# Kernel tuning notes

Measured on AMD Instinct MI355X. Metric: run time of the kernel, lower is better.

Reference implementation:

```python
import jax
import jax.numpy as jnp
import numpy as np
from jax import lax

KSIZE = 3
C = 32


def _conv3x3(x, w):
    # NCHW input, OIHW weight, stride 1, padding 1 (matches nn.Conv2d(padding=1))
    return lax.conv_general_dilated(
        x, w, window_strides=(1, 1), padding=((1, 1), (1, 1)),
        dimension_numbers=("NCHW", "OIHW", "NCHW"))


def setup_inputs() -> dict:
    key = jax.random.key(0)
    k1, k2, k3 = jax.random.split(key, 3)
    N, H, W = 2, 64, 64
    x = jax.random.normal(k1, (N, C, H, W), dtype=jnp.float32)
    # conv1: C -> C, 3x3; PyTorch default init scale ~ 1/sqrt(fan_in)
    conv1_w = jax.random.normal(k2, (C, C, 3, 3), dtype=jnp.float32) * (1.0 / np.sqrt(C * 9))
    # conv2: C -> C*C*9, 3x3
    conv2_w = jax.random.normal(k3, (C * C * KSIZE * KSIZE, C, 3, 3), dtype=jnp.float32) * (1.0 / np.sqrt(C * 9))
    return {"x": x, "conv1_w": conv1_w, "conv2_w": conv2_w}


def reference(x, conv1_w, conv2_w):
    N, _, H, W = x.shape
    # kernel-generation branch: conv -> relu -> conv -> tanh
    h = jax.nn.relu(_conv3x3(x, conv1_w))
    rst = _conv3x3(h, conv2_w)  # [N, C*C*9, H, W]
    weight = jnp.tanh(rst.reshape(N, C, C, H, W, KSIZE, KSIZE))
    # non-uniform conv apply: per-pixel CxC 3x3 kernel, pad=1
    xp = jnp.pad(x, ((0, 0), (0, 0), (1, 1), (1, 1)))
    # patches[n, ci, h, w, kh, kw] = xp[n, ci, h+kh, w+kw]
    patches = jnp.stack(
        [xp[:, :, kh:kh + H, kw:kw + W] for kh in range(KSIZE) for kw in range(KSIZE)],
        axis=-1).reshape(N, C, H, W, KSIZE, KSIZE)
    out = jnp.einsum("noihwkl,nihwkl->nohw", weight, patches)
    return out
```

## Files before the change

kernel.cpp:

```cpp
#include <hip/hip_runtime.h>

typedef unsigned int uint;
typedef unsigned short ushort_t;

#define CN 32
#define HW 4096
#define KDIM 288
#define PDIM 8192
#define NB 2

typedef __attribute__((ext_vector_type(8))) short bf16x8;
typedef __attribute__((ext_vector_type(4))) float f32x4;

static __device__ __forceinline__ ushort_t f2bf(float f) {
    uint u = __float_as_uint(f);
    uint r = (u + 0x7fffu + ((u >> 16) & 1u)) >> 16;
    return (ushort_t)r;
}

static __device__ __forceinline__ void gl_lds16(const void* g, void* l) {
    __builtin_amdgcn_global_load_lds(
        (const __attribute__((address_space(1))) unsigned int*)g,
        (__attribute__((address_space(3))) unsigned int*)l, 16, 0, 0);
}

static __device__ __forceinline__ float fast_tanh(float v) {
    float e = __expf(2.0f * v);
    return 1.0f - 2.0f * __builtin_amdgcn_rcpf(e + 1.0f);
}


__global__ __launch_bounds__(256) void prep_kernel(
    const float* __restrict__ x, const float* __restrict__ w1,
    const float* __restrict__ w2, float* __restrict__ hout,
    ushort_t* __restrict__ A_bf, float4* __restrict__ out_zero)
{
    __shared__ float w1s[KDIM];
    __shared__ float ps[2][128][4];
    int bb = blockIdx.x;
    int tid = threadIdx.x;
    if (bb < 512) {
        int n  = bb >> 8;
        int c  = (bb >> 3) & 31;
        int rg = bb & 7;
        for (int j = tid; j < KDIM; j += 256) w1s[j] = w1[c * KDIM + j];
        __syncthreads();

        int half = tid >> 7;
        int i2   = tid & 127;
        int hh   = rg * 8 + (i2 >> 4);
        int ws0  = (i2 & 15) * 4;

        float acc0 = 0.f, acc1 = 0.f, acc2 = 0.f, acc3 = 0.f;
        int ci0 = half * 16;
        for (int ci = ci0; ci < ci0 + 16; ci++) {
            const float* xp = x + (((size_t)(n * CN + ci)) << 12);
            #pragma unroll
            for (int kh = 0; kh < 3; kh++) {
                int y = hh + kh - 1;
                if ((unsigned)y >= 64u) continue;
                const float* row = xp + (y << 6);
                float4 v = *(const float4*)(row + ws0);
                float left  = (ws0 > 0)  ? row[ws0 - 1] : 0.f;
                float right = (ws0 < 60) ? row[ws0 + 4] : 0.f;
                float rb[6] = {left, v.x, v.y, v.z, v.w, right};
                const float* wp = &w1s[ci * 9 + kh * 3];
                #pragma unroll
                for (int kw = 0; kw < 3; kw++) {
                    float wgt = wp[kw];
                    acc0 = fmaf(wgt, rb[0 + kw], acc0);
                    acc1 = fmaf(wgt, rb[1 + kw], acc1);
                    acc2 = fmaf(wgt, rb[2 + kw], acc2);
                    acc3 = fmaf(wgt, rb[3 + kw], acc3);
                }
            }
        }
        ps[half][i2][0] = acc0; ps[half][i2][1] = acc1;
        ps[half][i2][2] = acc2; ps[half][i2][3] = acc3;
        __syncthreads();
        if (half == 0) {
            float4 o = make_float4(
                fmaxf(ps[0][i2][0] + ps[1][i2][0], 0.f),
                fmaxf(ps[0][i2][1] + ps[1][i2][1], 0.f),
                fmaxf(ps[0][i2][2] + ps[1][i2][2], 0.f),
                fmaxf(ps[0][i2][3] + ps[1][i2][3], 0.f));
            *(float4*)(hout + (((size_t)(n * CN + c)) << 12) + (hh << 6) + ws0) = o;
        }
    } else {
        int idx = (bb - 512) * 256 + tid;
        if (idx < 65536)
            out_zero[idx] = make_float4(0.f, 0.f, 0.f, 0.f);
        int row = idx / 36;
        int cw  = idx - row * 36;
        int g = cw >> 2, s = cw & 3;
        const float* base = w2 + (size_t)row * KDIM + g * 32;
        float4 lo = *(const float4*)(base + s * 4);
        float4 hi = *(const float4*)(base + 16 + s * 4);
        alignas(16) ushort_t o[8] = {f2bf(lo.x), f2bf(lo.y), f2bf(lo.z), f2bf(lo.w),
                                     f2bf(hi.x), f2bf(hi.y), f2bf(hi.z), f2bf(hi.w)};
        *(uint4*)(A_bf + (size_t)idx * 8) = *(const uint4*)o;
    }
}

__global__ __launch_bounds__(256) void im2col_bf16_perm(
    const float* __restrict__ h, ushort_t* __restrict__ Bm)
{
    int idx = blockIdx.x * 256 + threadIdx.x;
    int p  = idx / 36;
    int cw = idx - p * 36;
    int g = cw >> 2, s = cw & 3;
    int n  = p >> 12;
    int sp = p & 4095;
    int hh = sp >> 6;
    int w  = sp & 63;
    const float* hn = h + (((size_t)n * CN) << 12);
    alignas(16) ushort_t o[8];
    #pragma unroll
    for (int j = 0; j < 8; j++) {
        int ko = (j < 4) ? (s * 4 + j) : (12 + s * 4 + j);
        int k  = g * 32 + ko;
        int ci = (k * 57) >> 9;
        int kk = k - ci * 9;
        int kh = (kk * 11) >> 5;
        int kw = kk - kh * 3;
        int y  = hh + kh - 1;
        int xw = w + kw - 1;
        float v = 0.f;
        if ((unsigned)y < 64u && (unsigned)xw < 64u)
            v = hn[((size_t)ci << 12) + (y << 6) + xw];
        o[j] = f2bf(v);
    }
    *(uint4*)(Bm + (size_t)idx * 8) = *(const uint4*)o;
}

__global__ __launch_bounds__(512, 4) void fused_gemm_apply(
    const ushort_t* __restrict__ A, const ushort_t* __restrict__ B,
    const float* __restrict__ x, float* __restrict__ out)
{
    __shared__ ushort_t AL[3][128 * 32];
    __shared__ ushort_t BL[3][256 * 32];
    __shared__ float vred[4][256];

    int tid = threadIdx.x;
    int bid = blockIdx.x;
    int sb  = (bid & 7) * 288 + (bid >> 3);
    int tw  = sb % 144;
    int cg  = (sb / 144) & 7;
    int n   = sb / 1152;

    int lane = tid & 63, wv = tid >> 6;
    int wm = wv >> 2, wt = wv & 3;
    int i16 = lane & 15, kg = lane >> 4;

    int T0 = tw * 256;
    int c8 = T0 >> 12;
    int q0 = T0 & 4095;

    int cA = tid;
    int rA = cA >> 2;
    int k8A = (((cA & 3) ^ ((cA >> 3) & 3)) << 3);
    const ushort_t* srcA = A +
        (size_t)((cg * 4 + (rA >> 5)) * KDIM + (rA & 31) * 9 + c8) * KDIM + k8A;
    int cB0 = tid, cB1 = 512 + tid;
    int rB0 = cB0 >> 2, rB1 = cB1 >> 2;
    int k8B0 = (((cB0 & 3) ^ ((cB0 >> 3) & 3)) << 3);
    int k8B1 = (((cB1 & 3) ^ ((cB1 >> 3) & 3)) << 3);
    const ushort_t* srcB0 = B + (size_t)((n << 12) + q0 + rB0) * KDIM + k8B0;
    const ushort_t* srcB1 = B + (size_t)((n << 12) + q0 + rB1) * KDIM + k8B1;
    int dstA = wv * 512, dstB0 = wv * 512, dstB1 = 4096 + wv * 512;

#define STAGE(BUF, KS)                                                  \
    do { int _k0 = (KS) * 32;                                           \
        gl_lds16(srcA + _k0,  &AL[BUF][dstA]);                          \
        gl_lds16(srcB0 + _k0, &BL[BUF][dstB0]);                         \
        gl_lds16(srcB1 + _k0, &BL[BUF][dstB1]);                         \
    } while (0)

    f32x4 acc[4][4] = {};

    STAGE(0, 0);
    STAGE(1, 1);

    #pragma unroll
    for (int ks = 0; ks < 9; ks++) {
        int cur = ks % 3;
        if (ks < 7) {
            STAGE((ks + 2) % 3, ks + 2);
            __builtin_amdgcn_sched_barrier(0);
            asm volatile("s_waitcnt vmcnt(6)" ::: "memory");
        } else if (ks == 7) {
            __builtin_amdgcn_sched_barrier(0);
            asm volatile("s_waitcnt vmcnt(3)" ::: "memory");
        } else {
            __builtin_amdgcn_sched_barrier(0);
            asm volatile("s_waitcnt vmcnt(0)" ::: "memory");
        }
        __builtin_amdgcn_sched_barrier(0);
        __builtin_amdgcn_s_barrier();
        __builtin_amdgcn_sched_barrier(0);

        bf16x8 af[4], bfr[4];
        #pragma unroll
        for (int mf = 0; mf < 4; mf++) {
            int row = wm * 64 + mf * 16 + i16;
            af[mf] = *(const bf16x8*)
                &AL[cur][row * 32 + ((kg ^ ((row >> 1) & 3)) << 3)];
        }
        #pragma unroll
        for (int nf = 0; nf < 4; nf++) {
            int row = wt * 64 + nf * 16 + i16;
            bfr[nf] = *(const bf16x8*)
                &BL[cur][row * 32 + ((kg ^ ((row >> 1) & 3)) << 3)];
        }
        #pragma unroll
        for (int mf = 0; mf < 4; mf++)
            #pragma unroll
            for (int nf = 0; nf < 4; nf++)
                acc[mf][nf] = __builtin_amdgcn_mfma_f32_16x16x32_bf16(
                    af[mf], bfr[nf], acc[mf][nf], 0, 0, 0);

        __builtin_amdgcn_sched_barrier(0);
        asm volatile("s_waitcnt lgkmcnt(0)" ::: "memory");
        __builtin_amdgcn_sched_barrier(0);
        __builtin_amdgcn_s_barrier();
        __builtin_amdgcn_sched_barrier(0);
    }
#undef STAGE

    const float* xn = x + (((size_t)n * CN) << 12);
    #pragma unroll
    for (int nf = 0; nf < 4; nf++) {
        int t  = T0 + wt * 64 + nf * 16 + i16;
        uint sp = ((uint)t * 58255u) >> 19;
        int kk = t - (int)sp * 9;
        int kh = (kk * 11) >> 5;
        int kw = kk - kh * 3;
        int y  = (int)(sp >> 6) + kh - 1;
        int xw = (int)(sp & 63) + kw - 1;
        bool ok = ((unsigned)y < 64u) && ((unsigned)xw < 64u);
        int poff = (y << 6) + xw;
        float xa[4], xb[4];
        #pragma unroll
        for (int r = 0; r < 4; r++) {
            int cia = kg * 4 + r;
            xa[r] = ok ? xn[((size_t)cia << 12) + poff] : 0.f;
            xb[r] = ok ? xn[((size_t)(cia + 16) << 12) + poff] : 0.f;
        }
        float s0 = 0.f, s1 = 0.f;
        #pragma unroll
        for (int r = 0; r < 4; r++) {
            s0 = fmaf(fast_tanh(acc[0][nf][r]), xa[r], s0);
            s0 = fmaf(fast_tanh(acc[1][nf][r]), xb[r], s0);
            s1 = fmaf(fast_tanh(acc[2][nf][r]), xa[r], s1);
            s1 = fmaf(fast_tanh(acc[3][nf][r]), xb[r], s1);
        }
        s0 += __shfl_xor(s0, 16); s0 += __shfl_xor(s0, 32);
        s1 += __shfl_xor(s1, 16); s1 += __shfl_xor(s1, 32);
        if (kg == 0) {
            vred[2 * wm + 0][wt * 64 + nf * 16 + i16] = s0;
            vred[2 * wm + 1][wt * 64 + nf * 16 + i16] = s1;
        }
    }
    __syncthreads();

    if (tid < 128) {
        int g  = tid >> 5, bi = tid & 31;
        uint spA = ((uint)T0 * 58255u) >> 19;
        int sp = (int)spA + bi;
        int lo = sp * 9;     if (lo < T0) lo = T0;
        int hi = sp * 9 + 9; if (hi > T0 + 256) hi = T0 + 256;
        if (lo < hi) {
            float s = 0.f;
            for (int t = lo; t < hi; t++) s += vred[g][t - T0];
            atomicAdd(&out[(((size_t)n * CN + cg * 4 + g) << 12) + sp], s);
        }
    }
}

extern "C" void kernel_launch(void* const* d_in, const int* in_sizes, int n_in,
                              void* d_out, int out_size, void* d_ws, size_t ws_size,
                              hipStream_t stream) {
    const float* x  = (const float*)d_in[0];
    const float* w1 = (const float*)d_in[1];
    const float* w2 = (const float*)d_in[2];
    float* out = (float*)d_out;
    char* ws = (char*)d_ws;

    float*    hbuf  = (float*)ws;
    ushort_t* Bm_bf = (ushort_t*)(ws + 1048576u);
    ushort_t* A_bf  = (ushort_t*)(ws + 5767168u);

    hipLaunchKernelGGL(prep_kernel, dim3(1808), dim3(256), 0, stream,
                       x, w1, w2, hbuf, A_bf, (float4*)out);
    hipLaunchKernelGGL(im2col_bf16_perm, dim3(1152), dim3(256), 0,
                       stream, hbuf, Bm_bf);
    hipLaunchKernelGGL(fused_gemm_apply, dim3(2304), dim3(512), 0, stream,
                       A_bf, Bm_bf, x, out);
}
```

Baseline: 98.17 us.

## Restructure fused GEMM to 128x128 tiles with BK=64 split-phase double buffering

```diff
diff --git a/kernel.cpp b/kernel.cpp
--- a/kernel.cpp
+++ b/kernel.cpp
@@ -133,99 +133,159 @@
     *(uint4*)(Bm + (size_t)idx * 8) = *(const uint4*)o;
 }
 
-__global__ __launch_bounds__(512, 4) void fused_gemm_apply(
+__global__ __launch_bounds__(256) void fused_gemm_apply(
     const ushort_t* __restrict__ A, const ushort_t* __restrict__ B,
     const float* __restrict__ x, float* __restrict__ out)
 {
-    __shared__ ushort_t AL[3][128 * 32];
-    __shared__ ushort_t BL[3][256 * 32];
-    __shared__ float vred[4][256];
+    __shared__ ushort_t AL[2][128 * 64];
+    __shared__ ushort_t BL[2][128 * 64];
+    __shared__ float vred[4][128];
 
     int tid = threadIdx.x;
     int bid = blockIdx.x;
-    int sb  = (bid & 7) * 288 + (bid >> 3);
-    int tw  = sb % 144;
-    int cg  = (sb / 144) & 7;
-    int n   = sb / 1152;
+    int sb  = (bid & 7) * 576 + (bid >> 3);
+    int tw  = sb % 288;
+    int cg  = (sb / 288) & 7;
+    int n   = sb / 2304;
 
     int lane = tid & 63, wv = tid >> 6;
-    int wm = wv >> 2, wt = wv & 3;
+    int wm = wv >> 1, wt = wv & 1;
     int i16 = lane & 15, kg = lane >> 4;
 
-    int T0 = tw * 256;
+    int T0 = tw * 128;
     int c8 = T0 >> 12;
     int q0 = T0 & 4095;
 
-    int cA = tid;
-    int rA = cA >> 2;
-    int k8A = (((cA & 3) ^ ((cA >> 3) & 3)) << 3);
-    const ushort_t* srcA = A +
-        (size_t)((cg * 4 + (rA >> 5)) * KDIM + (rA & 31) * 9 + c8) * KDIM + k8A;
-    int cB0 = tid, cB1 = 512 + tid;
-    int rB0 = cB0 >> 2, rB1 = cB1 >> 2;
-    int k8B0 = (((cB0 & 3) ^ ((cB0 >> 3) & 3)) << 3);
-    int k8B1 = (((cB1 & 3) ^ ((cB1 >> 3) & 3)) << 3);
-    const ushort_t* srcB0 = B + (size_t)((n << 12) + q0 + rB0) * KDIM + k8B0;
-    const ushort_t* srcB1 = B + (size_t)((n << 12) + q0 + rB1) * KDIM + k8B1;
-    int dstA = wv * 512, dstB0 = wv * 512, dstB1 = 4096 + wv * 512;
-
-#define STAGE(BUF, KS)                                                  \
-    do { int _k0 = (KS) * 32;                                           \
-        gl_lds16(srcA + _k0,  &AL[BUF][dstA]);                          \
-        gl_lds16(srcB0 + _k0, &BL[BUF][dstB0]);                         \
-        gl_lds16(srcB1 + _k0, &BL[BUF][dstB1]);                         \
-    } while (0)
+    const ushort_t *sA[4], *sAt[4], *sB[4], *sBt[4];
+    #pragma unroll
+    for (int q = 0; q < 4; q++) {
+        int c = q * 256 + tid;
+        int r = c >> 3, s = c & 7;
+        int l = s ^ (r & 7);
+        int ofs  = ((l >> 2) << 5) + ((l & 3) << 3);
+        int ofsT = 256 + ((l & 3) << 3);
+        size_t aRow = (size_t)((cg * 4 + (r >> 5)) * KDIM + (r & 31) * 9 + c8);
+        sA[q]  = A + aRow * KDIM + ofs;
+        sAt[q] = A + aRow * KDIM + ofsT;
+        size_t bRow = (size_t)((n << 12) + q0 + r);
+        sB[q]  = B + bRow * KDIM + ofs;
+        sBt[q] = B + bRow * KDIM + ofsT;
+    }
+    int dstq[4];
+    #pragma unroll
+    for (int q = 0; q < 4; q++) dstq[q] = (q * 256 + wv * 64) * 8;
+
+#define SCHED0 __builtin_amdgcn_sched_barrier(0)
+#define RD_A(mf, kk) (*(const bf16x8*)&AL[cur][(wm * 64 + (mf) * 16 + i16) * 64 \
+        + (((((kk) << 2) + kg) ^ (i16 & 7)) << 3)])
+#define RD_B(nf, kk) (*(const bf16x8*)&BL[cur][(wt * 64 + (nf) * 16 + i16) * 64 \
+        + (((((kk) << 2) + kg) ^ (i16 & 7)) << 3)])
 
     f32x4 acc[4][4] = {};
 
-    STAGE(0, 0);
-    STAGE(1, 1);
-
-    #pragma unroll
-    for (int ks = 0; ks < 9; ks++) {
-        int cur = ks % 3;
-        if (ks < 7) {
-            STAGE((ks + 2) % 3, ks + 2);
-            __builtin_amdgcn_sched_barrier(0);
-            asm volatile("s_waitcnt vmcnt(6)" ::: "memory");
-        } else if (ks == 7) {
-            __builtin_amdgcn_sched_barrier(0);
-            asm volatile("s_waitcnt vmcnt(3)" ::: "memory");
+    #pragma unroll
+    for (int q = 0; q < 4; q++) {
+        gl_lds16(sA[q], &AL[0][dstq[q]]);
+        gl_lds16(sB[q], &BL[0][dstq[q]]);
+    }
+    SCHED0;
+    asm volatile("s_waitcnt vmcnt(0)" ::: "memory");
+    SCHED0;
+    __builtin_amdgcn_s_barrier();
+    SCHED0;
+
+    #pragma unroll
+    for (int it = 0; it < 4; it++) {
+        int cur = it & 1, nxt = cur ^ 1;
+        int ko = (it + 1) * 64;
+
+        if (it < 3) {
+            #pragma unroll
+            for (int q = 0; q < 4; q++) gl_lds16(sA[q] + ko, &AL[nxt][dstq[q]]);
         } else {
-            __builtin_amdgcn_sched_barrier(0);
+            #pragma unroll
+            for (int q = 0; q < 4; q++) gl_lds16(sAt[q], &AL[nxt][dstq[q]]);
+        }
+        {
+            bf16x8 af[4], bfr[4];
+            #pragma unroll
+            for (int mf = 0; mf < 4; mf++) af[mf] = RD_A(mf, 0);
+            #pragma unroll
+            for (int nf = 0; nf < 4; nf++) bfr[nf] = RD_B(nf, 0);
+            SCHED0;
+            __builtin_amdgcn_s_barrier();
+            SCHED0;
+            asm volatile("s_waitcnt lgkmcnt(0)" ::: "memory");
+            SCHED0;
+            __builtin_amdgcn_s_setprio(1);
+            #pragma unroll
+            for (int mf = 0; mf < 4; mf++)
+                #pragma unroll
+                for (int nf = 0; nf < 4; nf++)
+                    acc[mf][nf] = __builtin_amdgcn_mfma_f32_16x16x32_bf16(
+                        af[mf], bfr[nf], acc[mf][nf], 0, 0, 0);
+            __builtin_amdgcn_s_setprio(0);
+            SCHED0;
+            __builtin_amdgcn_s_barrier();
+            SCHED0;
+        }
+
+        if (it < 3) {
+            #pragma unroll
+            for (int q = 0; q < 4; q++) gl_lds16(sB[q] + ko, &BL[nxt][dstq[q]]);
+        } else {
+            #pragma unroll
+            for (int q = 0; q < 4; q++) gl_lds16(sBt[q], &BL[nxt][dstq[q]]);
+        }
+        {
+            bf16x8 af[4], bfr[4];
+            #pragma unroll
+            for (int mf = 0; mf < 4; mf++) af[mf] = RD_A(mf, 1);
+            #pragma unroll
+            for (int nf = 0; nf < 4; nf++) bfr[nf] = RD_B(nf, 1);
+            SCHED0;
+            __builtin_amdgcn_s_barrier();
+            SCHED0;
+            asm volatile("s_waitcnt lgkmcnt(0)" ::: "memory");
+            SCHED0;
+            __builtin_amdgcn_s_setprio(1);
+            #pragma unroll
+            for (int mf = 0; mf < 4; mf++)
+                #pragma unroll
+                for (int nf = 0; nf < 4; nf++)
+                    acc[mf][nf] = __builtin_amdgcn_mfma_f32_16x16x32_bf16(
+                        af[mf], bfr[nf], acc[mf][nf], 0, 0, 0);
+            __builtin_amdgcn_s_setprio(0);
+            SCHED0;
             asm volatile("s_waitcnt vmcnt(0)" ::: "memory");
-        }
-        __builtin_amdgcn_sched_barrier(0);
-        __builtin_amdgcn_s_barrier();
-        __builtin_amdgcn_sched_barrier(0);
-
+            SCHED0;
+            __builtin_amdgcn_s_barrier();
+            SCHED0;
+        }
+    }
+
+    {
+        int cur = 0;
         bf16x8 af[4], bfr[4];
         #pragma unroll
-        for (int mf = 0; mf < 4; mf++) {
-            int row = wm * 64 + mf * 16 + i16;
-            af[mf] = *(const bf16x8*)
-                &AL[cur][row * 32 + ((kg ^ ((row >> 1) & 3)) << 3)];
-        }
-        #pragma unroll
-        for (int nf = 0; nf < 4; nf++) {
-            int row = wt * 64 + nf * 16 + i16;
-            bfr[nf] = *(const bf16x8*)
-                &BL[cur][row * 32 + ((kg ^ ((row >> 1) & 3)) << 3)];
-        }
+        for (int mf = 0; mf < 4; mf++) af[mf] = RD_A(mf, 0);
+        #pragma unroll
+        for (int nf = 0; nf < 4; nf++) bfr[nf] = RD_B(nf, 0);
+        SCHED0;
+        asm volatile("s_waitcnt lgkmcnt(0)" ::: "memory");
+        SCHED0;
+        __builtin_amdgcn_s_setprio(1);
         #pragma unroll
         for (int mf = 0; mf < 4; mf++)
             #pragma unroll
             for (int nf = 0; nf < 4; nf++)
                 acc[mf][nf] = __builtin_amdgcn_mfma_f32_16x16x32_bf16(
                     af[mf], bfr[nf], acc[mf][nf], 0, 0, 0);
-
-        __builtin_amdgcn_sched_barrier(0);
-        asm volatile("s_waitcnt lgkmcnt(0)" ::: "memory");
-        __builtin_amdgcn_sched_barrier(0);
-        __builtin_amdgcn_s_barrier();
-        __builtin_amdgcn_sched_barrier(0);
-    }
-#undef STAGE
+        __builtin_amdgcn_s_setprio(0);
+    }
+#undef RD_A
+#undef RD_B
+#undef SCHED0
 
     const float* xn = x + (((size_t)n * CN) << 12);
     #pragma unroll
@@ -263,12 +323,12 @@
     }
     __syncthreads();
 
-    if (tid < 128) {
-        int g  = tid >> 5, bi = tid & 31;
+    if (tid < 64) {
+        int g  = tid >> 4, bi = tid & 15;
         uint spA = ((uint)T0 * 58255u) >> 19;
         int sp = (int)spA + bi;
         int lo = sp * 9;     if (lo < T0) lo = T0;
-        int hi = sp * 9 + 9; if (hi > T0 + 256) hi = T0 + 256;
+        int hi = sp * 9 + 9; if (hi > T0 + 128) hi = T0 + 128;
         if (lo < hi) {
             float s = 0.f;
             for (int t = lo; t < hi; t++) s += vred[g][t - T0];
@@ -294,6 +354,6 @@
                        x, w1, w2, hbuf, A_bf, (float4*)out);
     hipLaunchKernelGGL(im2col_bf16_perm, dim3(1152), dim3(256), 0,
                        stream, hbuf, Bm_bf);
-    hipLaunchKernelGGL(fused_gemm_apply, dim3(2304), dim3(512), 0, stream,
+    hipLaunchKernelGGL(fused_gemm_apply, dim3(4608), dim3(256), 0, stream,
                        A_bf, Bm_bf, x, out);
 }
```

New measurement: 119.1 us. 1.21x slower.
